# Performance work log

Hardware: AMD Instinct MI355X
Metric: run time of the kernel (lower is better)

Reference implementation:

```python
import jax, jax.numpy as jnp
import numpy as np

C_IN = 128      # pair channel
C_HID = 32      # per-head hidden dim
H = 4           # heads
INF = 1e9
LN_EPS = 1e-5


def setup_inputs() -> dict:
    key = jax.random.key(0)
    ks = jax.random.split(key, 8)
    B, N = 1, 256
    s = 0.02
    return {
        "x": jax.random.normal(ks[0], (B, N, N, C_IN), dtype=jnp.float32),
        "mask": jnp.ones((B, N, N), dtype=jnp.float32),
        "ln_w": jnp.ones((C_IN,), dtype=jnp.float32),
        "ln_b": jnp.zeros((C_IN,), dtype=jnp.float32),
        "w_b": jax.random.normal(ks[1], (H, C_IN), dtype=jnp.float32) * s,      # triangle-bias linear (no bias)
        "w_q": jax.random.normal(ks[2], (H * C_HID, C_IN), dtype=jnp.float32) * s,
        "w_k": jax.random.normal(ks[3], (H * C_HID, C_IN), dtype=jnp.float32) * s,
        "w_v": jax.random.normal(ks[4], (H * C_HID, C_IN), dtype=jnp.float32) * s,
        "w_g": jax.random.normal(ks[5], (H * C_HID, C_IN), dtype=jnp.float32) * s,
        "b_g": jnp.ones((H * C_HID,), dtype=jnp.float32),
        "w_o": jax.random.normal(ks[6], (C_IN, H * C_HID), dtype=jnp.float32) * s,
        "b_o": jnp.zeros((C_IN,), dtype=jnp.float32),
    }


def reference(x, mask, ln_w, ln_b, w_b, w_q, w_k, w_v, w_g, b_g, w_o, b_o):
    # starting=True -> no transpose
    # LayerNorm over channel dim
    mu = jnp.mean(x, axis=-1, keepdims=True)
    var = jnp.var(x, axis=-1, keepdims=True)
    xn = (x - mu) * jax.lax.rsqrt(var + LN_EPS) * ln_w + ln_b            # [B,I,J,C]

    # mask bias: [B, I, 1, 1, J]
    mask_bias = (INF * (mask - 1.0))[..., :, None, None, :]

    # triangle bias: linear -> [B,I,J,H] -> permute -> [B,H,I,J] -> [B,1,H,I,J]
    tri_bias = jnp.einsum("bijc,hc->bhij", xn, w_b)[:, None]

    # QKV projections, per-head: weights reshaped to [H, D, C]
    Wq = w_q.reshape(H, C_HID, C_IN)
    Wk = w_k.reshape(H, C_HID, C_IN)
    Wv = w_v.reshape(H, C_HID, C_IN)
    scale = 1.0 / np.sqrt(C_HID)
    q = jnp.einsum("bijc,hdc->bihjd", xn, Wq) * scale                    # [B,I,H,J,D]
    k = jnp.einsum("bijc,hdc->bihjd", xn, Wk)
    v = jnp.einsum("bijc,hdc->bihjd", xn, Wv)

    # attention over the J (column) axis of each row i
    a = jnp.einsum("bihqd,bihkd->bihqk", q, k) + mask_bias + tri_bias    # [B,I,H,J,J]
    a = jax.nn.softmax(a, axis=-1)
    o = jnp.einsum("bihqk,bihkd->biqhd", a, v)                           # [B,I,J,H,D]

    # sigmoid gating
    g = jax.nn.sigmoid(jnp.einsum("bijc,ec->bije", xn, w_g) + b_g)       # [B,I,J,H*D]
    o = o.reshape(*o.shape[:-2], H * C_HID) * g

    # output projection
    return jnp.einsum("bije,ce->bijc", o, w_o) + b_o                     # [B,I,J,C_in]
```

## Files before the change

### kernel.cpp

```cpp
#include <hip/hip_runtime.h>

#define N 256
#define C 128
#define H 4
#define D 32
#define NP (N*N)
#define INFV 1e9f
#define LN_EPS 1e-5f

#define PSTR 264

using f32x4 = __attribute__((ext_vector_type(4))) float;
using bf8   = __attribute__((ext_vector_type(8))) short;

__device__ __forceinline__ float bf2f(ushort u) {
    union { uint u; float f; } v; v.u = ((uint)u) << 16; return v.f;
}
__device__ __forceinline__ ushort f2bf(float f) {
    union { float f; uint u; } v; v.f = f;
    uint u = v.u;
    u += 0x7fffu + ((u >> 16) & 1u);
    return (ushort)(u >> 16);
}
__device__ __forceinline__ ushort f2bf_trunc(float f) {
    union { float f; uint u; } v; v.f = f;
    return (ushort)(v.u >> 16);
}

__global__ __launch_bounds__(256) void prep_weights(
    const float* __restrict__ wq, const float* __restrict__ wk,
    const float* __restrict__ wv, const float* __restrict__ wg,
    const float* __restrict__ wb, const float* __restrict__ wo,
    ushort* __restrict__ Wcat, ushort* __restrict__ Wb, ushort* __restrict__ Wo)
{
    int t = blockIdx.x * 256 + threadIdx.x;
    const float scale = 0.17677669529663689f;
    float v;
    if (t < 16384)       v = wq[t] * scale;
    else if (t < 32768)  v = wk[t - 16384];
    else if (t < 49152)  v = wv[t - 32768];
    else                 v = wg[t - 49152];
    Wcat[t] = f2bf(v);
    if (t < 16384) Wo[t] = f2bf(wo[t]);
    if (t < 512)   Wb[t] = f2bf(wb[t]);
}

__global__ __launch_bounds__(256) void ln_kernel(
    const float* __restrict__ x, const float* __restrict__ lnw,
    const float* __restrict__ lnb, ushort* __restrict__ xn)
{
    int wave = threadIdx.x >> 6, lane = threadIdx.x & 63;
    int p = blockIdx.x * 4 + wave;
    const float* xp = x + (size_t)p * C;
    float a0 = xp[lane], a1 = xp[lane + 64];
    float s = a0 + a1, ss = a0 * a0 + a1 * a1;
    #pragma unroll
    for (int m = 1; m < 64; m <<= 1) {
        s  += __shfl_xor(s, m, 64);
        ss += __shfl_xor(ss, m, 64);
    }
    float mean = s * (1.f / 128.f);
    float var  = ss * (1.f / 128.f) - mean * mean;
    float rstd = rsqrtf(var + LN_EPS);
    ushort* op = xn + (size_t)p * C;
    op[lane]      = f2bf((a0 - mean) * rstd * lnw[lane]      + lnb[lane]);
    op[lane + 64] = f2bf((a1 - mean) * rstd * lnw[lane + 64] + lnb[lane + 64]);
}

__global__ __launch_bounds__(256) void tri_kernel(
    const ushort* __restrict__ xn, const ushort* __restrict__ Wb,
    ushort* __restrict__ tri_p)
{
    __shared__ float wb[512];
    int t = threadIdx.x;
    wb[t]       = bf2f(Wb[t]);
    wb[t + 256] = bf2f(Wb[t + 256]);
    __syncthreads();
    int p = blockIdx.x * 256 + t;
    const ushort* xp = xn + (size_t)p * C;
    float acc0 = 0, acc1 = 0, acc2 = 0, acc3 = 0;
    #pragma unroll
    for (int c8 = 0; c8 < 16; c8++) {
        uint4 pk = ((const uint4*)xp)[c8];
        const ushort* u = (const ushort*)&pk;
        #pragma unroll
        for (int j = 0; j < 8; j++) {
            float xv = bf2f(u[j]);
            int c = c8 * 8 + j;
            acc0 += xv * wb[c];
            acc1 += xv * wb[128 + c];
            acc2 += xv * wb[256 + c];
            acc3 += xv * wb[384 + c];
        }
    }
    int q = p >> 8, k = p & 255;
    int qc = q >> 4, quad = (q >> 2) & 3, r = q & 3;
    int n = k >> 4, lrow = k & 15;
    int lane = quad * 16 + lrow;
    int v = n * 4 + r, j = v >> 3, m = v & 7;
    int base = ((qc * 8 + j) * 64 + lane) * 8 + m;
    tri_p[base]             = f2bf(acc0);
    tri_p[65536 + base]     = f2bf(acc1);
    tri_p[2 * 65536 + base] = f2bf(acc2);
    tri_p[3 * 65536 + base] = f2bf(acc3);
}

__global__ __launch_bounds__(256, 2) void proj_gemm(
    const ushort* __restrict__ xn, const ushort* __restrict__ Wcat,
    const float* __restrict__ bg,
    ushort* __restrict__ qb, ushort* __restrict__ kb,
    ushort* __restrict__ vb, ushort* __restrict__ gate)
{
    __shared__ ushort At[128 * 128];
    __shared__ ushort Bt[128 * 128];
    int mt = blockIdx.x;
    int nt = blockIdx.y;
    int t  = threadIdx.x;

    const uint4* Ag = (const uint4*)(xn   + (size_t)mt * 128 * C);
    const uint4* Bg = (const uint4*)(Wcat + (size_t)nt * 128 * C);
    #pragma unroll
    for (int ii = 0; ii < 8; ii++) {
        int idx = t + ii * 256;
        ((uint4*)At)[idx] = Ag[idx];
        ((uint4*)Bt)[idx] = Bg[idx];
    }
    __syncthreads();

    int wave = t >> 6, lane = t & 63;
    int lrow = lane & 15, quad = lane >> 4;
    int wr = wave >> 1, wc = wave & 1;

    f32x4 acc[4][4];
    #pragma unroll
    for (int mi = 0; mi < 4; mi++)
        #pragma unroll
        for (int ni = 0; ni < 4; ni++) acc[mi][ni] = (f32x4){0.f, 0.f, 0.f, 0.f};

    #pragma unroll
    for (int ks = 0; ks < 4; ks++) {
        bf8 a[4], b[4];
        #pragma unroll
        for (int mi = 0; mi < 4; mi++)
            a[mi] = *(const bf8*)&At[(wr * 64 + mi * 16 + lrow) * 128 + ks * 32 + quad * 8];
        #pragma unroll
        for (int ni = 0; ni < 4; ni++)
            b[ni] = *(const bf8*)&Bt[(wc * 64 + ni * 16 + lrow) * 128 + ks * 32 + quad * 8];
        #pragma unroll
        for (int mi = 0; mi < 4; mi++)
            #pragma unroll
            for (int ni = 0; ni < 4; ni++)
                acc[mi][ni] = __builtin_amdgcn_mfma_f32_16x16x32_bf16(a[mi], b[ni], acc[mi][ni], 0, 0, 0);
    }

    ushort* dst = (nt == 0) ? qb : (nt == 1) ? kb : (nt == 2) ? vb : gate;
    bool gated = (nt == 3);
    #pragma unroll
    for (int mi = 0; mi < 4; mi++) {
        #pragma unroll
        for (int ni = 0; ni < 4; ni++) {
            int col = wc * 64 + ni * 16 + lrow;
            #pragma unroll
            for (int r = 0; r < 4; r++) {
                int row = mt * 128 + wr * 64 + mi * 16 + quad * 4 + r;
                float v = acc[mi][ni][r];
                if (gated) v = 1.f / (1.f + __expf(-(v + bg[col])));
                dst[(size_t)row * C + col] = f2bf(v);
            }
        }
    }
}

__global__ __launch_bounds__(256, 3) void attn_kernel(
    const ushort* __restrict__ qb, const ushort* __restrict__ kb,
    const ushort* __restrict__ vb, const ushort* __restrict__ tri_p,
    const float* __restrict__ mask, ushort* __restrict__ ob)
{
    __shared__ ushort Vt[32 * PSTR];
    __shared__ ushort Pl[4][16 * PSTR];

    int i  = blockIdx.x;
    int h  = blockIdx.y;
    int t  = threadIdx.x;
    int wave = t >> 6, lane = t & 63;
    int lrow = lane & 15, quad = lane >> 4;

    {
        const ushort* vp = vb + ((size_t)(i * N + t)) * C + h * D;
        #pragma unroll
        for (int d = 0; d < D; d++) Vt[d * PSTR + t] = vp[d];
    }
    bf8 kf[16];
    #pragma unroll
    for (int n = 0; n < 16; n++)
        kf[n] = *(const bf8*)(kb + ((size_t)(i * N + n * 16 + lrow)) * C + h * D + quad * 8);
    float mb[16];
    #pragma unroll
    for (int n = 0; n < 16; n++)
        mb[n] = INFV * (mask[i * N + n * 16 + lrow] - 1.0f);
    __syncthreads();

    ushort* Pw = &Pl[wave][0];
    const ushort* trih = tri_p + (size_t)h * 65536;

    #pragma unroll 1
    for (int c = 0; c < 4; c++) {
        int qc = wave * 4 + c;
        bf8 aq = *(const bf8*)(qb + ((size_t)(i * N + qc * 16 + lrow)) * C + h * D + quad * 8);
        float sum[4] = {0.f, 0.f, 0.f, 0.f};

        #pragma unroll
        for (int half = 0; half < 2; half++) {
            f32x4 s8[8];
            #pragma unroll
            for (int n8 = 0; n8 < 8; n8++)
                s8[n8] = __builtin_amdgcn_mfma_f32_16x16x32_bf16(
                    aq, kf[half * 8 + n8], (f32x4){0.f, 0.f, 0.f, 0.f}, 0, 0, 0);

            const ushort* tp = trih + ((size_t)(qc * 8 + half * 4) * 64 + lane) * 8;
            bf8 tf[4];
            #pragma unroll
            for (int jj = 0; jj < 4; jj++)
                tf[jj] = *(const bf8*)(tp + jj * 512);

            #pragma unroll
            for (int n8 = 0; n8 < 8; n8++) {
                int n = half * 8 + n8;
                #pragma unroll
                for (int r = 0; r < 4; r++) {
                    float tb = bf2f(((const ushort*)&tf[n8 >> 1])[((n8 & 1) << 2) + r]);
                    float e  = __expf(s8[n8][r] + tb + mb[n]);
                    sum[r]  += e;
                    Pw[(quad * 4 + r) * PSTR + n * 16 + lrow] = f2bf_trunc(e);
                }
            }
        }
        #pragma unroll
        for (int r = 0; r < 4; r++) {
            float s = sum[r];
            s += __shfl_xor(s, 1, 64);
            s += __shfl_xor(s, 2, 64);
            s += __shfl_xor(s, 4, 64);
            s += __shfl_xor(s, 8, 64);
            sum[r] = 1.f / s;
        }
        __asm__ volatile("s_waitcnt lgkmcnt(0)" ::: "memory");

        f32x4 o[2];
        o[0] = (f32x4){0.f, 0.f, 0.f, 0.f};
        o[1] = (f32x4){0.f, 0.f, 0.f, 0.f};
        #pragma unroll
        for (int ks = 0; ks < 8; ks++) {
            bf8 ap = *(const bf8*)&Pw[lrow * PSTR + ks * 32 + quad * 8];
            #pragma unroll
            for (int nv = 0; nv < 2; nv++) {
                bf8 bv = *(const bf8*)&Vt[(nv * 16 + lrow) * PSTR + ks * 32 + quad * 8];
                o[nv] = __builtin_amdgcn_mfma_f32_16x16x32_bf16(ap, bv, o[nv], 0, 0, 0);
            }
        }
        #pragma unroll
        for (int nv = 0; nv < 2; nv++) {
            int d = nv * 16 + lrow;
            #pragma unroll
            for (int r = 0; r < 4; r++) {
                int qg = qc * 16 + quad * 4 + r;
                ob[((size_t)(i * N + qg)) * C + h * D + d] = f2bf(o[nv][r] * sum[r]);
            }
        }
    }
}

__global__ __launch_bounds__(256, 2) void out_gemm(
    const ushort* __restrict__ ob, const ushort* __restrict__ gate,
    const ushort* __restrict__ Wo, const float* __restrict__ bo,
    float* __restrict__ out)
{
    __shared__ ushort At[128 * 128];
    __shared__ ushort Bt[128 * 128];
    int mt = blockIdx.x;
    int t  = threadIdx.x;

    const uint4* Og = (const uint4*)(ob   + (size_t)mt * 128 * C);
    const uint4* Gg = (const uint4*)(gate + (size_t)mt * 128 * C);
    const uint4* Bg = (const uint4*)Wo;
    #pragma unroll
    for (int ii = 0; ii < 8; ii++) {
        int idx = t + ii * 256;
        uint4 o4 = Og[idx], g4 = Gg[idx], r4;
        const ushort* os = (const ushort*)&o4;
        const ushort* gs = (const ushort*)&g4;
        ushort* rs = (ushort*)&r4;
        #pragma unroll
        for (int j = 0; j < 8; j++) rs[j] = f2bf(bf2f(os[j]) * bf2f(gs[j]));
        ((uint4*)At)[idx] = r4;
        ((uint4*)Bt)[idx] = Bg[idx];
    }
    __syncthreads();

    int wave = t >> 6, lane = t & 63;
    int lrow = lane & 15, quad = lane >> 4;
    int wr = wave >> 1, wc = wave & 1;

    f32x4 acc[4][4];
    #pragma unroll
    for (int mi = 0; mi < 4; mi++)
        #pragma unroll
        for (int ni = 0; ni < 4; ni++) acc[mi][ni] = (f32x4){0.f, 0.f, 0.f, 0.f};

    #pragma unroll
    for (int ks = 0; ks < 4; ks++) {
        bf8 a[4], b[4];
        #pragma unroll
        for (int mi = 0; mi < 4; mi++)
            a[mi] = *(const bf8*)&At[(wr * 64 + mi * 16 + lrow) * 128 + ks * 32 + quad * 8];
        #pragma unroll
        for (int ni = 0; ni < 4; ni++)
            b[ni] = *(const bf8*)&Bt[(wc * 64 + ni * 16 + lrow) * 128 + ks * 32 + quad * 8];
        #pragma unroll
        for (int mi = 0; mi < 4; mi++)
            #pragma unroll
            for (int ni = 0; ni < 4; ni++)
                acc[mi][ni] = __builtin_amdgcn_mfma_f32_16x16x32_bf16(a[mi], b[ni], acc[mi][ni], 0, 0, 0);
    }

    #pragma unroll
    for (int mi = 0; mi < 4; mi++) {
        #pragma unroll
        for (int ni = 0; ni < 4; ni++) {
            int col = wc * 64 + ni * 16 + lrow;
            float bias = bo[col];
            #pragma unroll
            for (int r = 0; r < 4; r++) {
                int row = mt * 128 + wr * 64 + mi * 16 + quad * 4 + r;
                out[(size_t)row * C + col] = acc[mi][ni][r] + bias;
            }
        }
    }
}

extern "C" void kernel_launch(void* const* d_in, const int* in_sizes, int n_in,
                              void* d_out, int out_size, void* d_ws, size_t ws_size,
                              hipStream_t stream)
{
    const float* x    = (const float*)d_in[0];
    const float* mask = (const float*)d_in[1];
    const float* lnw  = (const float*)d_in[2];
    const float* lnb  = (const float*)d_in[3];
    const float* wb   = (const float*)d_in[4];
    const float* wq   = (const float*)d_in[5];
    const float* wk   = (const float*)d_in[6];
    const float* wv   = (const float*)d_in[7];
    const float* wg   = (const float*)d_in[8];
    const float* bg   = (const float*)d_in[9];
    const float* wo   = (const float*)d_in[10];
    const float* bo   = (const float*)d_in[11];
    float* out = (float*)d_out;

    uintptr_t w = (uintptr_t)d_ws;
    ushort* xn    = (ushort*)w; w += (size_t)NP * C * 2;
    ushort* qb    = (ushort*)w; w += (size_t)NP * C * 2;
    ushort* kb    = (ushort*)w; w += (size_t)NP * C * 2;
    ushort* vb    = (ushort*)w; w += (size_t)NP * C * 2;
    ushort* gate  = (ushort*)w; w += (size_t)NP * C * 2;
    ushort* ob    = (ushort*)w; w += (size_t)NP * C * 2;
    ushort* tri_p = (ushort*)w; w += (size_t)H * NP * 2;
    ushort* Wcat  = (ushort*)w; w += 512 * 128 * 2;
    ushort* Wb    = (ushort*)w; w += 512 * 2;
    ushort* Wo    = (ushort*)w; w += 128 * 128 * 2;

    prep_weights<<<256, 256, 0, stream>>>(wq, wk, wv, wg, wb, wo, Wcat, Wb, Wo);
    ln_kernel<<<NP / 4, 256, 0, stream>>>(x, lnw, lnb, xn);
    tri_kernel<<<NP / 256, 256, 0, stream>>>(xn, Wb, tri_p);
    proj_gemm<<<dim3(NP / 128, 4), 256, 0, stream>>>(xn, Wcat, bg, qb, kb, vb, gate);
    attn_kernel<<<dim3(N, H), 256, 0, stream>>>(qb, kb, vb, tri_p, mask, ob);
    out_gemm<<<NP / 128, 256, 0, stream>>>(ob, gate, Wo, bo, out);
}
```

Before: 198.4 us.

## Transpose V in projection, read weights/K/V from global, fold log2e into exp2

The projection GEMM now runs all four output tiles in one block so the xn tile is loaded into LDS once. It writes V pre-transposed per (row, head), which lets attention read V and K fragments straight from global memory instead of staging them in LDS and registers. Weight tiles are also read from global rather than LDS, and log2e is folded into the Q scale, tri-bias and mask so the softmax can use exp2f. LDS and register use drop and occupancy bounds rise to 4, but more global/L2 traffic now sits on the MFMA critical path and the projection grid is four times smaller.

```diff
diff --git a/kernel.cpp b/kernel.cpp
--- a/kernel.cpp
+++ b/kernel.cpp
@@ -5,10 +5,10 @@
 #define H 4
 #define D 32
 #define NP (N*N)
-#define INFV 1e9f
 #define LN_EPS 1e-5f
 
 #define PSTR 264
+#define LOG2E 1.4426950408889634f
 
 using f32x4 = __attribute__((ext_vector_type(4))) float;
 using bf8   = __attribute__((ext_vector_type(8))) short;
@@ -34,7 +34,7 @@
     ushort* __restrict__ Wcat, ushort* __restrict__ Wb, ushort* __restrict__ Wo)
 {
     int t = blockIdx.x * 256 + threadIdx.x;
-    const float scale = 0.17677669529663689f;
+    const float scale = 0.17677669529663689f * LOG2E;
     float v;
     if (t < 16384)       v = wq[t] * scale;
     else if (t < 32768)  v = wk[t - 16384];
@@ -99,84 +99,101 @@
     int lane = quad * 16 + lrow;
     int v = n * 4 + r, j = v >> 3, m = v & 7;
     int base = ((qc * 8 + j) * 64 + lane) * 8 + m;
-    tri_p[base]             = f2bf(acc0);
-    tri_p[65536 + base]     = f2bf(acc1);
-    tri_p[2 * 65536 + base] = f2bf(acc2);
-    tri_p[3 * 65536 + base] = f2bf(acc3);
-}
-
-__global__ __launch_bounds__(256, 2) void proj_gemm(
+    tri_p[base]             = f2bf(acc0 * LOG2E);
+    tri_p[65536 + base]     = f2bf(acc1 * LOG2E);
+    tri_p[2 * 65536 + base] = f2bf(acc2 * LOG2E);
+    tri_p[3 * 65536 + base] = f2bf(acc3 * LOG2E);
+}
+
+__global__ __launch_bounds__(256, 4) void proj_gemm(
     const ushort* __restrict__ xn, const ushort* __restrict__ Wcat,
     const float* __restrict__ bg,
     ushort* __restrict__ qb, ushort* __restrict__ kb,
-    ushort* __restrict__ vb, ushort* __restrict__ gate)
+    ushort* __restrict__ vbT, ushort* __restrict__ gate)
 {
     __shared__ ushort At[128 * 128];
-    __shared__ ushort Bt[128 * 128];
     int mt = blockIdx.x;
-    int nt = blockIdx.y;
     int t  = threadIdx.x;
 
-    const uint4* Ag = (const uint4*)(xn   + (size_t)mt * 128 * C);
-    const uint4* Bg = (const uint4*)(Wcat + (size_t)nt * 128 * C);
+    const uint4* Ag = (const uint4*)(xn + (size_t)mt * 128 * C);
     #pragma unroll
     for (int ii = 0; ii < 8; ii++) {
         int idx = t + ii * 256;
         ((uint4*)At)[idx] = Ag[idx];
-        ((uint4*)Bt)[idx] = Bg[idx];
     }
     __syncthreads();
 
     int wave = t >> 6, lane = t & 63;
     int lrow = lane & 15, quad = lane >> 4;
     int wr = wave >> 1, wc = wave & 1;
-
-    f32x4 acc[4][4];
-    #pragma unroll
-    for (int mi = 0; mi < 4; mi++)
-        #pragma unroll
-        for (int ni = 0; ni < 4; ni++) acc[mi][ni] = (f32x4){0.f, 0.f, 0.f, 0.f};
-
-    #pragma unroll
-    for (int ks = 0; ks < 4; ks++) {
-        bf8 a[4], b[4];
+    int i_row = mt >> 1;
+
+    #pragma unroll 1
+    for (int nt = 0; nt < 4; nt++) {
+        f32x4 acc[4][4];
         #pragma unroll
         for (int mi = 0; mi < 4; mi++)
-            a[mi] = *(const bf8*)&At[(wr * 64 + mi * 16 + lrow) * 128 + ks * 32 + quad * 8];
-        #pragma unroll
-        for (int ni = 0; ni < 4; ni++)
-            b[ni] = *(const bf8*)&Bt[(wc * 64 + ni * 16 + lrow) * 128 + ks * 32 + quad * 8];
-        #pragma unroll
-        for (int mi = 0; mi < 4; mi++)
+            #pragma unroll
+            for (int ni = 0; ni < 4; ni++) acc[mi][ni] = (f32x4){0.f, 0.f, 0.f, 0.f};
+
+        const ushort* Wbase = Wcat + (size_t)(nt * 128 + wc * 64) * C + quad * 8;
+        #pragma unroll
+        for (int ks = 0; ks < 4; ks++) {
+            bf8 a[4], b[4];
+            #pragma unroll
+            for (int mi = 0; mi < 4; mi++)
+                a[mi] = *(const bf8*)&At[(wr * 64 + mi * 16 + lrow) * 128 + ks * 32 + quad * 8];
             #pragma unroll
             for (int ni = 0; ni < 4; ni++)
-                acc[mi][ni] = __builtin_amdgcn_mfma_f32_16x16x32_bf16(a[mi], b[ni], acc[mi][ni], 0, 0, 0);
-    }
-
-    ushort* dst = (nt == 0) ? qb : (nt == 1) ? kb : (nt == 2) ? vb : gate;
-    bool gated = (nt == 3);
-    #pragma unroll
-    for (int mi = 0; mi < 4; mi++) {
-        #pragma unroll
-        for (int ni = 0; ni < 4; ni++) {
-            int col = wc * 64 + ni * 16 + lrow;
-            #pragma unroll
-            for (int r = 0; r < 4; r++) {
-                int row = mt * 128 + wr * 64 + mi * 16 + quad * 4 + r;
-                float v = acc[mi][ni][r];
-                if (gated) v = 1.f / (1.f + __expf(-(v + bg[col])));
-                dst[(size_t)row * C + col] = f2bf(v);
-            }
-        }
-    }
-}
-
-__global__ __launch_bounds__(256, 3) void attn_kernel(
+                b[ni] = *(const bf8*)(Wbase + (size_t)(ni * 16 + lrow) * C + ks * 32);
+            #pragma unroll
+            for (int mi = 0; mi < 4; mi++)
+                #pragma unroll
+                for (int ni = 0; ni < 4; ni++)
+                    acc[mi][ni] = __builtin_amdgcn_mfma_f32_16x16x32_bf16(a[mi], b[ni], acc[mi][ni], 0, 0, 0);
+        }
+
+        if (nt == 2) {
+            #pragma unroll
+            for (int mi = 0; mi < 4; mi++) {
+                int j0 = (mt & 1) * 128 + wr * 64 + mi * 16 + quad * 4;
+                #pragma unroll
+                for (int ni = 0; ni < 4; ni++) {
+                    int col = wc * 64 + ni * 16 + lrow;
+                    ushort4 pk;
+                    pk.x = f2bf(acc[mi][ni][0]);
+                    pk.y = f2bf(acc[mi][ni][1]);
+                    pk.z = f2bf(acc[mi][ni][2]);
+                    pk.w = f2bf(acc[mi][ni][3]);
+                    *(ushort4*)&vbT[((size_t)(i_row * H) * D + col) * N + j0] = pk;
+                }
+            }
+        } else {
+            ushort* dst = (nt == 0) ? qb : (nt == 1) ? kb : gate;
+            bool gated = (nt == 3);
+            #pragma unroll
+            for (int mi = 0; mi < 4; mi++) {
+                #pragma unroll
+                for (int ni = 0; ni < 4; ni++) {
+                    int col = wc * 64 + ni * 16 + lrow;
+                    #pragma unroll
+                    for (int r = 0; r < 4; r++) {
+                        int row = mt * 128 + wr * 64 + mi * 16 + quad * 4 + r;
+                        float v = acc[mi][ni][r];
+                        if (gated) v = 1.f / (1.f + __expf(-(v + bg[col])));
+                        dst[(size_t)row * C + col] = f2bf(v);
+                    }
+                }
+            }
+        }
+    }
+}
+
+__global__ __launch_bounds__(256, 4) void attn_kernel(
     const ushort* __restrict__ qb, const ushort* __restrict__ kb,
-    const ushort* __restrict__ vb, const ushort* __restrict__ tri_p,
+    const ushort* __restrict__ vbT, const ushort* __restrict__ tri_p,
     const float* __restrict__ mask, ushort* __restrict__ ob)
 {
-    __shared__ ushort Vt[32 * PSTR];
     __shared__ ushort Pl[4][16 * PSTR];
 
     int i  = blockIdx.x;
@@ -185,38 +202,31 @@
     int wave = t >> 6, lane = t & 63;
     int lrow = lane & 15, quad = lane >> 4;
 
-    {
-        const ushort* vp = vb + ((size_t)(i * N + t)) * C + h * D;
-        #pragma unroll
-        for (int d = 0; d < D; d++) Vt[d * PSTR + t] = vp[d];
-    }
-    bf8 kf[16];
+    float mb[16];
     #pragma unroll
     for (int n = 0; n < 16; n++)
-        kf[n] = *(const bf8*)(kb + ((size_t)(i * N + n * 16 + lrow)) * C + h * D + quad * 8);
-    float mb[16];
-    #pragma unroll
-    for (int n = 0; n < 16; n++)
-        mb[n] = INFV * (mask[i * N + n * 16 + lrow] - 1.0f);
-    __syncthreads();
+        mb[n] = (1e9f * LOG2E) * (mask[i * N + n * 16 + lrow] - 1.0f);
 
     ushort* Pw = &Pl[wave][0];
-    const ushort* trih = tri_p + (size_t)h * 65536;
+    const ushort* trih  = tri_p + (size_t)h * 65536;
+    const ushort* kbase = kb  + (size_t)(i * N) * C + h * D + quad * 8;
+    const ushort* vbase = vbT + (size_t)((i * H + h) * D) * N + quad * 8;
 
     #pragma unroll 1
     for (int c = 0; c < 4; c++) {
         int qc = wave * 4 + c;
-        bf8 aq = *(const bf8*)(qb + ((size_t)(i * N + qc * 16 + lrow)) * C + h * D + quad * 8);
+        bf8 aq = *(const bf8*)(qb + (size_t)(i * N + qc * 16 + lrow) * C + h * D + quad * 8);
         float sum[4] = {0.f, 0.f, 0.f, 0.f};
 
         #pragma unroll
         for (int half = 0; half < 2; half++) {
             f32x4 s8[8];
             #pragma unroll
-            for (int n8 = 0; n8 < 8; n8++)
+            for (int n8 = 0; n8 < 8; n8++) {
+                bf8 kf = *(const bf8*)(kbase + (size_t)((half * 8 + n8) * 16 + lrow) * C);
                 s8[n8] = __builtin_amdgcn_mfma_f32_16x16x32_bf16(
-                    aq, kf[half * 8 + n8], (f32x4){0.f, 0.f, 0.f, 0.f}, 0, 0, 0);
-
+                    aq, kf, (f32x4){0.f, 0.f, 0.f, 0.f}, 0, 0, 0);
+            }
             const ushort* tp = trih + ((size_t)(qc * 8 + half * 4) * 64 + lane) * 8;
             bf8 tf[4];
             #pragma unroll
@@ -229,7 +239,7 @@
                 #pragma unroll
                 for (int r = 0; r < 4; r++) {
                     float tb = bf2f(((const ushort*)&tf[n8 >> 1])[((n8 & 1) << 2) + r]);
-                    float e  = __expf(s8[n8][r] + tb + mb[n]);
+                    float e  = exp2f(s8[n8][r] + tb + mb[n]);
                     sum[r]  += e;
                     Pw[(quad * 4 + r) * PSTR + n * 16 + lrow] = f2bf_trunc(e);
                 }
@@ -254,7 +264,7 @@
             bf8 ap = *(const bf8*)&Pw[lrow * PSTR + ks * 32 + quad * 8];
             #pragma unroll
             for (int nv = 0; nv < 2; nv++) {
-                bf8 bv = *(const bf8*)&Vt[(nv * 16 + lrow) * PSTR + ks * 32 + quad * 8];
+                bf8 bv = *(const bf8*)(vbase + (size_t)(nv * 16 + lrow) * N + ks * 32);
                 o[nv] = __builtin_amdgcn_mfma_f32_16x16x32_bf16(ap, bv, o[nv], 0, 0, 0);
             }
         }
@@ -264,25 +274,23 @@
             #pragma unroll
             for (int r = 0; r < 4; r++) {
                 int qg = qc * 16 + quad * 4 + r;
-                ob[((size_t)(i * N + qg)) * C + h * D + d] = f2bf(o[nv][r] * sum[r]);
-            }
-        }
-    }
-}
-
-__global__ __launch_bounds__(256, 2) void out_gemm(
+                ob[(size_t)(i * N + qg) * C + h * D + d] = f2bf(o[nv][r] * sum[r]);
+            }
+        }
+    }
+}
+
+__global__ __launch_bounds__(256, 4) void out_gemm(
     const ushort* __restrict__ ob, const ushort* __restrict__ gate,
     const ushort* __restrict__ Wo, const float* __restrict__ bo,
     float* __restrict__ out)
 {
     __shared__ ushort At[128 * 128];
-    __shared__ ushort Bt[128 * 128];
     int mt = blockIdx.x;
     int t  = threadIdx.x;
 
     const uint4* Og = (const uint4*)(ob   + (size_t)mt * 128 * C);
     const uint4* Gg = (const uint4*)(gate + (size_t)mt * 128 * C);
-    const uint4* Bg = (const uint4*)Wo;
     #pragma unroll
     for (int ii = 0; ii < 8; ii++) {
         int idx = t + ii * 256;
@@ -293,7 +301,6 @@
         #pragma unroll
         for (int j = 0; j < 8; j++) rs[j] = f2bf(bf2f(os[j]) * bf2f(gs[j]));
         ((uint4*)At)[idx] = r4;
-        ((uint4*)Bt)[idx] = Bg[idx];
     }
     __syncthreads();
 
@@ -307,6 +314,7 @@
         #pragma unroll
         for (int ni = 0; ni < 4; ni++) acc[mi][ni] = (f32x4){0.f, 0.f, 0.f, 0.f};
 
+    const ushort* Wbase = Wo + (size_t)(wc * 64) * C + quad * 8;
     #pragma unroll
     for (int ks = 0; ks < 4; ks++) {
         bf8 a[4], b[4];
@@ -315,7 +323,7 @@
             a[mi] = *(const bf8*)&At[(wr * 64 + mi * 16 + lrow) * 128 + ks * 32 + quad * 8];
         #pragma unroll
         for (int ni = 0; ni < 4; ni++)
-            b[ni] = *(const bf8*)&Bt[(wc * 64 + ni * 16 + lrow) * 128 + ks * 32 + quad * 8];
+            b[ni] = *(const bf8*)(Wbase + (size_t)(ni * 16 + lrow) * C + ks * 32);
         #pragma unroll
         for (int mi = 0; mi < 4; mi++)
             #pragma unroll
@@ -360,7 +368,7 @@
     ushort* xn    = (ushort*)w; w += (size_t)NP * C * 2;
     ushort* qb    = (ushort*)w; w += (size_t)NP * C * 2;
     ushort* kb    = (ushort*)w; w += (size_t)NP * C * 2;
-    ushort* vb    = (ushort*)w; w += (size_t)NP * C * 2;
+    ushort* vbT   = (ushort*)w; w += (size_t)NP * C * 2;
     ushort* gate  = (ushort*)w; w += (size_t)NP * C * 2;
     ushort* ob    = (ushort*)w; w += (size_t)NP * C * 2;
     ushort* tri_p = (ushort*)w; w += (size_t)H * NP * 2;
@@ -371,7 +379,7 @@
     prep_weights<<<256, 256, 0, stream>>>(wq, wk, wv, wg, wb, wo, Wcat, Wb, Wo);
     ln_kernel<<<NP / 4, 256, 0, stream>>>(x, lnw, lnb, xn);
     tri_kernel<<<NP / 256, 256, 0, stream>>>(xn, Wb, tri_p);
-    proj_gemm<<<dim3(NP / 128, 4), 256, 0, stream>>>(xn, Wcat, bg, qb, kb, vb, gate);
-    attn_kernel<<<dim3(N, H), 256, 0, stream>>>(qb, kb, vb, tri_p, mask, ob);
+    proj_gemm<<<NP / 128, 256, 0, stream>>>(xn, Wcat, bg, qb, kb, vbT, gate);
+    attn_kernel<<<dim3(N, H), 256, 0, stream>>>(qb, kb, vbT, tri_p, mask, ob);
     out_gemm<<<NP / 128, 256, 0, stream>>>(ob, gate, Wo, bo, out);
 }
```

Result: slower. 283.8 us (+43.1%).
